# Kernel tuning notes

Hardware: AMD Instinct MI355X
Metric: run time of the kernel (lower is better)

## Reference

```python
import jax, jax.numpy as jnp
import numpy as np

B, S, D, H = 8, 8192, 256, 256


def setup_inputs() -> dict:
    key = jax.random.key(0)
    ks = jax.random.split(key, 5)
    scale = 1.0 / np.sqrt(D)  # mimic nn.Linear init scale
    return {
        "x": jax.random.normal(ks[0], (B, S, D), dtype=jnp.float32),
        "h0": jnp.zeros((B, 1, H), dtype=jnp.float32),
        "w_h_w": jax.random.normal(ks[1], (H, D), dtype=jnp.float32) * scale,
        "w_h_b": jax.random.normal(ks[2], (H,), dtype=jnp.float32) * scale,
        "w_z_w": jax.random.normal(ks[3], (H, D), dtype=jnp.float32) * scale,
        "w_z_b": jax.random.normal(ks[4], (H,), dtype=jnp.float32) * scale,
    }


def reference(x, h0, w_h_w, w_h_b, w_z_w, w_z_b):
    # Projections over the whole sequence (same math as per-step Linear calls)
    z = jax.nn.sigmoid(jnp.einsum('bsd,hd->bsh', x, w_z_w) + w_z_b)  # [B,S,H]
    h_tilde = jnp.einsum('bsd,hd->bsh', x, w_h_w) + w_h_b            # [B,S,H]

    def step(h_prev, zh):
        z_t, ht_t = zh  # each [B,H]
        h_t = (1.0 - z_t) * h_prev + z_t * ht_t
        return h_t, h_t

    # scan over time axis; carry is [B,H]
    _, hs = jax.lax.scan(step, h0[:, 0],
                         (jnp.swapaxes(z, 0, 1), jnp.swapaxes(h_tilde, 0, 1)))
    return jnp.swapaxes(hs, 0, 1)  # [B,S,H]
```

## Files before the change

kernel.cpp:

```cpp
#include <hip/hip_runtime.h>
#include <math.h>


constexpr int B_ = 8;
constexpr int S_ = 8192;
constexpr int D_ = 256;
constexpr int H_ = 256;
constexpr int M_ = B_ * S_;
constexpr int CHUNKS = 128;
constexpr int CLEN = S_ / CHUNKS;

typedef __attribute__((ext_vector_type(8))) short bf16x8;
typedef __attribute__((ext_vector_type(4))) float f32x4;

__device__ __forceinline__ uint pack2bf(float f0, float f1) {
  const uint u0 = __float_as_uint(f0) + 0x8000u;
  const uint u1 = __float_as_uint(f1) + 0x8000u;
  return __builtin_amdgcn_perm(u1, u0, 0x07060302u);
}

__global__ __launch_bounds__(256) void gemm_zh(
    const float* __restrict__ x,
    const float* __restrict__ whw, const float* __restrict__ whb,
    const float* __restrict__ wzw, const float* __restrict__ wzb,
    uint* __restrict__ ab)
{
  __shared__ ushort xs[128][72];
  __shared__ ushort wzs[64][72];
  __shared__ ushort whs[64][72];

  const int tid = threadIdx.x;
  const int g    = blockIdx.x;
  const int xcd  = g & 7;
  const int loc  = g >> 3;
  const int nt   = loc & 3;
  const int panel = (loc >> 2) * 8 + xcd;
  const int m0 = panel * 128;
  const int n0 = nt * 64;

  const int lane = tid & 63;
  const int w  = tid >> 6;
  const int mb = (w & 1) * 64;
  const int nb = (w >> 1) * 32;
  const int q  = lane >> 4;
  const int cn = lane & 15;

  f32x4 accz[4][2] = {};
  f32x4 acch[4][2] = {};

  for (int k0 = 0; k0 < D_; k0 += 64) {
    __syncthreads();
#pragma unroll
    for (int f = 0; f < 8; f++) {
      const int idx = tid + 256 * f;
      const int row = idx >> 4, seg = idx & 15;
      float4 v = *(const float4*)(x + (size_t)(m0 + row) * D_ + k0 + seg * 4);
      *(uint2*)&xs[row][seg * 4] =
          make_uint2(pack2bf(v.x, v.y), pack2bf(v.z, v.w));
    }
#pragma unroll
    for (int f = 0; f < 4; f++) {
      const int idx = tid + 256 * f;
      const int row = idx >> 4, seg = idx & 15;
      float4 vz = *(const float4*)(wzw + (size_t)(n0 + row) * D_ + k0 + seg * 4);
      float4 vh = *(const float4*)(whw + (size_t)(n0 + row) * D_ + k0 + seg * 4);
      *(uint2*)&wzs[row][seg * 4] =
          make_uint2(pack2bf(vz.x, vz.y), pack2bf(vz.z, vz.w));
      *(uint2*)&whs[row][seg * 4] =
          make_uint2(pack2bf(vh.x, vh.y), pack2bf(vh.z, vh.w));
    }
    __syncthreads();
#pragma unroll
    for (int ks = 0; ks < 2; ks++) {
      const int kk = ks * 32 + q * 8;
      bf16x8 af[4], bz[2], bh[2];
#pragma unroll
      for (int i = 0; i < 4; i++)
        af[i] = *(const bf16x8*)&xs[mb + i * 16 + cn][kk];
#pragma unroll
      for (int j = 0; j < 2; j++) {
        bz[j] = *(const bf16x8*)&wzs[nb + j * 16 + cn][kk];
        bh[j] = *(const bf16x8*)&whs[nb + j * 16 + cn][kk];
      }
#pragma unroll
      for (int i = 0; i < 4; i++)
#pragma unroll
        for (int j = 0; j < 2; j++) {
          accz[i][j] = __builtin_amdgcn_mfma_f32_16x16x32_bf16(af[i], bz[j], accz[i][j], 0, 0, 0);
          acch[i][j] = __builtin_amdgcn_mfma_f32_16x16x32_bf16(af[i], bh[j], acch[i][j], 0, 0, 0);
        }
    }
  }

#pragma unroll
  for (int j = 0; j < 2; j++) {
    const int ch = n0 + nb + j * 16 + cn;
    const float zb = wzb[ch], hb = whb[ch];
#pragma unroll
    for (int i = 0; i < 4; i++) {
#pragma unroll
      for (int r = 0; r < 4; r++) {
        const int row = m0 + mb + i * 16 + q * 4 + r;
        const float zpre = accz[i][j][r] + zb;
        const float hpre = acch[i][j][r] + hb;
        const float e = __expf(-zpre);
        const float rcp = __builtin_amdgcn_rcpf(1.0f + e);
        ab[(size_t)row * H_ + ch] = pack2bf(e * rcp, hpre * rcp);
      }
    }
  }
}

__global__ __launch_bounds__(256) void scan_phaseA(
    const uint* __restrict__ ab,
    float* __restrict__ P_out, float* __restrict__ Q_out)
{
  const int c = blockIdx.x;
  const int b = blockIdx.y;
  const int ch = threadIdx.x;
  size_t base = ((size_t)b * S_ + (size_t)c * CLEN) * H_ + ch;
  float P = 1.f, Q = 0.f;
  for (int t0 = 0; t0 < CLEN; t0 += 8) {
    uint v[8];
#pragma unroll
    for (int j = 0; j < 8; j++)
      v[j] = ab[base + (size_t)(t0 + j) * H_];
#pragma unroll
    for (int j = 0; j < 8; j++) {
      const float a = __uint_as_float(v[j] << 16);
      const float bb = __uint_as_float(v[j] & 0xFFFF0000u);
      Q = fmaf(a, Q, bb);
      P *= a;
    }
  }
  const size_t idx = ((size_t)b * CHUNKS + c) * H_ + ch;
  P_out[idx] = P;
  Q_out[idx] = Q;
}

__global__ __launch_bounds__(256) void scan_phaseB(
    const float* __restrict__ h0in, const float* __restrict__ P,
    const float* __restrict__ Q, float* __restrict__ hstate)
{
  const int b = blockIdx.x;
  const int h = threadIdx.x;
  const size_t base = (size_t)b * CHUNKS * H_ + h;
  float hc = h0in[(size_t)b * H_ + h];
  for (int c0 = 0; c0 < CHUNKS; c0 += 8) {
    float p[8], q[8];
#pragma unroll
    for (int j = 0; j < 8; j++) {
      p[j] = P[base + (size_t)(c0 + j) * H_];
      q[j] = Q[base + (size_t)(c0 + j) * H_];
    }
#pragma unroll
    for (int j = 0; j < 8; j++) {
      hstate[base + (size_t)(c0 + j) * H_] = hc;
      hc = fmaf(p[j], hc, q[j]);
    }
  }
}

__global__ __launch_bounds__(256) void scan_phaseC(
    const uint* __restrict__ ab, const float* __restrict__ hstate,
    float* __restrict__ out)
{
  const int c = blockIdx.x;
  const int b = blockIdx.y;
  const int ch = threadIdx.x;
  size_t base = ((size_t)b * S_ + (size_t)c * CLEN) * H_ + ch;
  float hc = hstate[((size_t)b * CHUNKS + c) * H_ + ch];
  for (int t0 = 0; t0 < CLEN; t0 += 8) {
    uint v[8];
#pragma unroll
    for (int j = 0; j < 8; j++)
      v[j] = ab[base + (size_t)(t0 + j) * H_];
#pragma unroll
    for (int j = 0; j < 8; j++) {
      const float a = __uint_as_float(v[j] << 16);
      const float bb = __uint_as_float(v[j] & 0xFFFF0000u);
      hc = fmaf(a, hc, bb);
      out[base + (size_t)(t0 + j) * H_] = hc;
    }
  }
}

extern "C" void kernel_launch(void* const* d_in, const int* in_sizes, int n_in,
                              void* d_out, int out_size, void* d_ws, size_t ws_size,
                              hipStream_t stream) {
  const float* x   = (const float*)d_in[0];
  const float* h0  = (const float*)d_in[1];
  const float* whw = (const float*)d_in[2];
  const float* whb = (const float*)d_in[3];
  const float* wzw = (const float*)d_in[4];
  const float* wzb = (const float*)d_in[5];
  float* out = (float*)d_out;

  uint*  ab     = (uint*)d_ws;
  float* chunkP = (float*)(ab + (size_t)M_ * H_);
  float* chunkQ = chunkP + (size_t)B_ * CHUNKS * H_;
  float* hstate = chunkQ + (size_t)B_ * CHUNKS * H_;

  gemm_zh<<<(M_ / 128) * 4, 256, 0, stream>>>(x, whw, whb, wzw, wzb, ab);
  scan_phaseA<<<dim3(CHUNKS, B_), 256, 0, stream>>>(ab, chunkP, chunkQ);
  scan_phaseB<<<B_, 256, 0, stream>>>(h0, chunkP, chunkQ, hstate);
  scan_phaseC<<<dim3(CHUNKS, B_), 256, 0, stream>>>(ab, hstate, out);
}
```

Measured before the change: 192.8 us.

## Fuse three scan phases into one cooperative kernel keeping chunk data in registers

Replaces the three scan kernels with a single cooperative launch. Each block loads its 64-step chunk of packed gate/candidate values into registers once, computes the chunk's carry coefficients, runs the cross-chunk prefix in a few blocks after a grid sync, then reuses the register-held values to write outputs after a second grid sync. This removes the second full read of the intermediate buffer and two kernel launches. In exchange it adds two grid-wide barriers and heavy register use, and it needs all 1024 blocks to be resident at once, otherwise it falls back to the original three kernels.

```diff
diff --git a/kernel.cpp b/kernel.cpp
--- a/kernel.cpp
+++ b/kernel.cpp
@@ -1,4 +1,5 @@
 #include <hip/hip_runtime.h>
+#include <hip/hip_cooperative_groups.h>
 #include <math.h>
 
 
@@ -108,6 +109,69 @@
         ab[(size_t)row * H_ + ch] = pack2bf(e * rcp, hpre * rcp);
       }
     }
+  }
+}
+
+__global__ __launch_bounds__(256, 4) void scan_fused(
+    const uint* __restrict__ ab, const float* __restrict__ h0in,
+    float* __restrict__ chunkP, float* __restrict__ chunkQ,
+    float* __restrict__ hstate, float* __restrict__ out)
+{
+  const int blk = blockIdx.x;
+  const int b = blk >> 7;
+  const int c = blk & (CHUNKS - 1);
+  const int ch = threadIdx.x;
+  const size_t base = ((size_t)b * S_ + (size_t)c * CLEN) * H_ + ch;
+  const size_t cidx = ((size_t)b * CHUNKS + c) * H_ + ch;
+
+  uint v[CLEN];
+#pragma unroll
+  for (int t = 0; t < CLEN; t++)
+    v[t] = ab[base + (size_t)t * H_];
+
+  float P = 1.f, Q = 0.f;
+#pragma unroll
+  for (int t = 0; t < CLEN; t++) {
+    const float a  = __uint_as_float(v[t] << 16);
+    const float bb = __uint_as_float(v[t] & 0xFFFF0000u);
+    Q = fmaf(a, Q, bb);
+    P *= a;
+  }
+  chunkP[cidx] = P;
+  chunkQ[cidx] = Q;
+
+  __threadfence();
+  cooperative_groups::this_grid().sync();
+
+  if (blk < B_) {
+    const int b2 = blk;
+    const size_t base2 = (size_t)b2 * CHUNKS * H_ + ch;
+    float hc = h0in[(size_t)b2 * H_ + ch];
+    for (int c0 = 0; c0 < CHUNKS; c0 += 8) {
+      float p[8], q[8];
+#pragma unroll
+      for (int j = 0; j < 8; j++) {
+        p[j] = chunkP[base2 + (size_t)(c0 + j) * H_];
+        q[j] = chunkQ[base2 + (size_t)(c0 + j) * H_];
+      }
+#pragma unroll
+      for (int j = 0; j < 8; j++) {
+        hstate[base2 + (size_t)(c0 + j) * H_] = hc;
+        hc = fmaf(p[j], hc, q[j]);
+      }
+    }
+  }
+
+  __threadfence();
+  cooperative_groups::this_grid().sync();
+
+  float hc = hstate[cidx];
+#pragma unroll
+  for (int t = 0; t < CLEN; t++) {
+    const float a  = __uint_as_float(v[t] << 16);
+    const float bb = __uint_as_float(v[t] & 0xFFFF0000u);
+    hc = fmaf(a, hc, bb);
+    out[base + (size_t)t * H_] = hc;
   }
 }
 
@@ -202,7 +266,15 @@
   float* hstate = chunkQ + (size_t)B_ * CHUNKS * H_;
 
   gemm_zh<<<(M_ / 128) * 4, 256, 0, stream>>>(x, whw, whb, wzw, wzb, ab);
-  scan_phaseA<<<dim3(CHUNKS, B_), 256, 0, stream>>>(ab, chunkP, chunkQ);
-  scan_phaseB<<<B_, 256, 0, stream>>>(h0, chunkP, chunkQ, hstate);
-  scan_phaseC<<<dim3(CHUNKS, B_), 256, 0, stream>>>(ab, hstate, out);
-}
+
+  const uint* ab_c = ab;
+  void* cargs[6] = {(void*)&ab_c, (void*)&h0, (void*)&chunkP,
+                    (void*)&chunkQ, (void*)&hstate, (void*)&out};
+  hipError_t err = hipLaunchCooperativeKernel(
+      scan_fused, dim3(CHUNKS * B_), dim3(256), cargs, 0, stream);
+  if (err != hipSuccess) {
+    scan_phaseA<<<dim3(CHUNKS, B_), 256, 0, stream>>>(ab, chunkP, chunkQ);
+    scan_phaseB<<<B_, 256, 0, stream>>>(h0, chunkP, chunkQ, hstate);
+    scan_phaseC<<<dim3(CHUNKS, B_), 256, 0, stream>>>(ab, hstate, out);
+  }
+}
```

Measured after the change: 586.7 us. 204% more time.

## Fuse chunk-summary scan into GEMM epilogue and drop separate phase-A kernel

Applied to the files above, without the earlier changes.

The GEMM epilogue now computes each 64-step chunk's composed affine (P,Q) summary directly from its register tile, using a serial combine over the four rows per lane plus cross-lane shuffles, and writes it as a float2. This removes the scan_phaseA kernel, which re-read the whole packed z/h buffer from memory, along with one launch. Phase B reads the interleaved float2 summaries, and phases B and C are unrolled further to keep more loads in flight. In exchange the GEMM epilogue carries extra register and shuffle work.

```diff
diff --git a/kernel.cpp b/kernel.cpp
--- a/kernel.cpp
+++ b/kernel.cpp
@@ -23,7 +23,7 @@
     const float* __restrict__ x,
     const float* __restrict__ whw, const float* __restrict__ whb,
     const float* __restrict__ wzw, const float* __restrict__ wzb,
-    uint* __restrict__ ab)
+    uint* __restrict__ ab, float2* __restrict__ chunkPQ)
 {
   __shared__ ushort xs[128][72];
   __shared__ ushort wzs[64][72];
@@ -92,10 +92,15 @@
     }
   }
 
+  const int row0 = m0 + mb;
+  const int bb2  = row0 >> 13;
+  const int cc   = (row0 & 8191) >> 6;
+
 #pragma unroll
   for (int j = 0; j < 2; j++) {
     const int ch = n0 + nb + j * 16 + cn;
     const float zb = wzb[ch], hb = whb[ch];
+    uint u[4][4];
 #pragma unroll
     for (int i = 0; i < 4; i++) {
 #pragma unroll
@@ -105,58 +110,69 @@
         const float hpre = acch[i][j][r] + hb;
         const float e = __expf(-zpre);
         const float rcp = __builtin_amdgcn_rcpf(1.0f + e);
-        ab[(size_t)row * H_ + ch] = pack2bf(e * rcp, hpre * rcp);
-      }
-    }
-  }
-}
-
-__global__ __launch_bounds__(256) void scan_phaseA(
-    const uint* __restrict__ ab,
-    float* __restrict__ P_out, float* __restrict__ Q_out)
-{
-  const int c = blockIdx.x;
-  const int b = blockIdx.y;
-  const int ch = threadIdx.x;
-  size_t base = ((size_t)b * S_ + (size_t)c * CLEN) * H_ + ch;
-  float P = 1.f, Q = 0.f;
-  for (int t0 = 0; t0 < CLEN; t0 += 8) {
-    uint v[8];
-#pragma unroll
-    for (int j = 0; j < 8; j++)
-      v[j] = ab[base + (size_t)(t0 + j) * H_];
-#pragma unroll
-    for (int j = 0; j < 8; j++) {
-      const float a = __uint_as_float(v[j] << 16);
-      const float bb = __uint_as_float(v[j] & 0xFFFF0000u);
-      Q = fmaf(a, Q, bb);
-      P *= a;
-    }
-  }
-  const size_t idx = ((size_t)b * CHUNKS + c) * H_ + ch;
-  P_out[idx] = P;
-  Q_out[idx] = Q;
+        const uint pk = pack2bf(e * rcp, hpre * rcp);
+        ab[(size_t)row * H_ + ch] = pk;
+        u[i][r] = pk;
+      }
+    }
+    float P[4], Q[4];
+#pragma unroll
+    for (int i = 0; i < 4; i++) {
+      float Pi = 1.f, Qi = 0.f;
+#pragma unroll
+      for (int r = 0; r < 4; r++) {
+        const float a  = __uint_as_float(u[i][r] << 16);
+        const float bv = __uint_as_float(u[i][r] & 0xFFFF0000u);
+        Qi = fmaf(a, Qi, bv);
+        Pi *= a;
+      }
+      P[i] = Pi; Q[i] = Qi;
+    }
+#pragma unroll
+    for (int i = 0; i < 4; i++) {
+      {
+        const float Pp = __shfl_xor(P[i], 16);
+        const float Qp = __shfl_xor(Q[i], 16);
+        const bool later = (lane & 16) != 0;
+        Q[i] = later ? fmaf(P[i], Qp, Q[i]) : fmaf(Pp, Q[i], Qp);
+        P[i] = P[i] * Pp;
+      }
+      {
+        const float Pp = __shfl_xor(P[i], 32);
+        const float Qp = __shfl_xor(Q[i], 32);
+        const bool later = (lane & 32) != 0;
+        Q[i] = later ? fmaf(P[i], Qp, Q[i]) : fmaf(Pp, Q[i], Qp);
+        P[i] = P[i] * Pp;
+      }
+    }
+    float Pc = P[0], Qc = Q[0];
+#pragma unroll
+    for (int i = 1; i < 4; i++) {
+      Qc = fmaf(P[i], Qc, Q[i]);
+      Pc *= P[i];
+    }
+    if (lane < 16)
+      chunkPQ[((size_t)bb2 * CHUNKS + cc) * H_ + ch] = make_float2(Pc, Qc);
+  }
 }
 
 __global__ __launch_bounds__(256) void scan_phaseB(
-    const float* __restrict__ h0in, const float* __restrict__ P,
-    const float* __restrict__ Q, float* __restrict__ hstate)
+    const float* __restrict__ h0in, const float2* __restrict__ pq,
+    float* __restrict__ hstate)
 {
   const int b = blockIdx.x;
   const int h = threadIdx.x;
   const size_t base = (size_t)b * CHUNKS * H_ + h;
   float hc = h0in[(size_t)b * H_ + h];
-  for (int c0 = 0; c0 < CHUNKS; c0 += 8) {
-    float p[8], q[8];
-#pragma unroll
-    for (int j = 0; j < 8; j++) {
-      p[j] = P[base + (size_t)(c0 + j) * H_];
-      q[j] = Q[base + (size_t)(c0 + j) * H_];
-    }
-#pragma unroll
-    for (int j = 0; j < 8; j++) {
+  for (int c0 = 0; c0 < CHUNKS; c0 += 16) {
+    float2 v[16];
+#pragma unroll
+    for (int j = 0; j < 16; j++)
+      v[j] = pq[base + (size_t)(c0 + j) * H_];
+#pragma unroll
+    for (int j = 0; j < 16; j++) {
       hstate[base + (size_t)(c0 + j) * H_] = hc;
-      hc = fmaf(p[j], hc, q[j]);
+      hc = fmaf(v[j].x, hc, v[j].y);
     }
   }
 }
@@ -170,14 +186,15 @@
   const int ch = threadIdx.x;
   size_t base = ((size_t)b * S_ + (size_t)c * CLEN) * H_ + ch;
   float hc = hstate[((size_t)b * CHUNKS + c) * H_ + ch];
-  for (int t0 = 0; t0 < CLEN; t0 += 8) {
-    uint v[8];
-#pragma unroll
-    for (int j = 0; j < 8; j++)
+#pragma unroll
+  for (int t0 = 0; t0 < CLEN; t0 += 16) {
+    uint v[16];
+#pragma unroll
+    for (int j = 0; j < 16; j++)
       v[j] = ab[base + (size_t)(t0 + j) * H_];
 #pragma unroll
-    for (int j = 0; j < 8; j++) {
-      const float a = __uint_as_float(v[j] << 16);
+    for (int j = 0; j < 16; j++) {
+      const float a  = __uint_as_float(v[j] << 16);
       const float bb = __uint_as_float(v[j] & 0xFFFF0000u);
       hc = fmaf(a, hc, bb);
       out[base + (size_t)(t0 + j) * H_] = hc;
@@ -196,13 +213,11 @@
   const float* wzb = (const float*)d_in[5];
   float* out = (float*)d_out;
 
-  uint*  ab     = (uint*)d_ws;
-  float* chunkP = (float*)(ab + (size_t)M_ * H_);
-  float* chunkQ = chunkP + (size_t)B_ * CHUNKS * H_;
-  float* hstate = chunkQ + (size_t)B_ * CHUNKS * H_;
-
-  gemm_zh<<<(M_ / 128) * 4, 256, 0, stream>>>(x, whw, whb, wzw, wzb, ab);
-  scan_phaseA<<<dim3(CHUNKS, B_), 256, 0, stream>>>(ab, chunkP, chunkQ);
-  scan_phaseB<<<B_, 256, 0, stream>>>(h0, chunkP, chunkQ, hstate);
+  uint*   ab      = (uint*)d_ws;
+  float2* chunkPQ = (float2*)(ab + (size_t)M_ * H_);
+  float*  hstate  = (float*)(chunkPQ + (size_t)B_ * CHUNKS * H_);
+
+  gemm_zh<<<(M_ / 128) * 4, 256, 0, stream>>>(x, whw, whb, wzw, wzb, ab, chunkPQ);
+  scan_phaseB<<<B_, 256, 0, stream>>>(h0, (const float2*)chunkPQ, hstate);
   scan_phaseC<<<dim3(CHUNKS, B_), 256, 0, stream>>>(ab, hstate, out);
 }
```

New measurement: 181.9 us. 1.06x faster.
